# Kernel tuning notes

Measured on AMD Instinct MI355X. Metric: run time of the kernel, lower is better.

Reference implementation:

```python
import jax, jax.numpy as jnp
import numpy as np

B, S, H, I, G = 4, 2048, 2048, 8192, 128


def _onebit_quant(w, group_size):
    # Group-wise 1-bit (sign) quantization along the input dim with per-group
    # abs-mean scale, as in BitNet-style OneBitLinear.
    out_f, in_f = w.shape
    wg = w.reshape(out_f, in_f // group_size, group_size)
    scale = jnp.mean(jnp.abs(wg), axis=-1, keepdims=True)  # [out, n_groups, 1]
    wq = jnp.sign(wg) * scale
    return wq.reshape(out_f, in_f)


def setup_inputs() -> dict:
    key = jax.random.key(0)
    k1, k2, k3, k4 = jax.random.split(key, 4)
    return {
        "x": jax.random.normal(k1, (B, S, H), dtype=jnp.float32),
        "w_gate": jax.random.normal(k2, (I, H), dtype=jnp.float32) * 0.02,
        "w_up": jax.random.normal(k3, (I, H), dtype=jnp.float32) * 0.02,
        "w_down": jax.random.normal(k4, (H, I), dtype=jnp.float32) * 0.02,
        "group_size": G,
    }


def reference(x, w_gate, w_up, w_down, group_size):
    wg_q = _onebit_quant(w_gate, group_size)   # [I, H]
    wu_q = _onebit_quant(w_up, group_size)     # [I, H]
    wd_q = _onebit_quant(w_down, group_size)   # [H, I]
    gate = jnp.einsum('bsh,ih->bsi', x, wg_q)  # [B, S, I]
    up = jnp.einsum('bsh,ih->bsi', x, wu_q)    # [B, S, I]
    h = jax.nn.silu(gate) * up                 # [B, S, I]
    return jnp.einsum('bsi,hi->bsh', h, wd_q)  # [B, S, H]
```

## Files before the change

kernel.cpp:

```cpp
#include <hip/hip_runtime.h>
#include <hip/hip_bf16.h>
#include <cstdint>
#include <cstddef>

using bf16 = __hip_bfloat16;

typedef __attribute__((ext_vector_type(8))) short short8;
typedef __attribute__((ext_vector_type(4))) float f32x4;
typedef __attribute__((ext_vector_type(4))) unsigned short us4;

static constexpr int Bb = 4, Ss = 2048, Hh = 2048, Ii = 8192, Gg = 128;
static constexpr int Mm = Bb * Ss;

#define MEMFENCE() asm volatile("" ::: "memory")
#define BARRIER() do { MEMFENCE(); __builtin_amdgcn_s_barrier(); MEMFENCE(); } while (0)

__global__ void quant_onebit(const float* __restrict__ w, bf16* __restrict__ wq,
                             int ngroups) {
  int gid = blockIdx.x * 4 + (threadIdx.x >> 6);
  if (gid >= ngroups) return;
  int lane = threadIdx.x & 63;
  size_t base = (size_t)gid * Gg + (size_t)lane * 2;
  float2 v = *(const float2*)(w + base);
  float s = fabsf(v.x) + fabsf(v.y);
#pragma unroll
  for (int m = 32; m >= 1; m >>= 1) s += __shfl_xor(s, m);
  float scale = s * (1.0f / 128.0f);
  float q0 = (v.x > 0.f) ? scale : ((v.x < 0.f) ? -scale : 0.f);
  float q1 = (v.y > 0.f) ? scale : ((v.y < 0.f) ? -scale : 0.f);
  unsigned int p =
      (unsigned int)__builtin_bit_cast(unsigned short, __float2bfloat16(q0)) |
      ((unsigned int)__builtin_bit_cast(unsigned short, __float2bfloat16(q1)) << 16);
  *(unsigned int*)(wq + base) = p;
}

__global__ void cast_f32_bf16(const float* __restrict__ in, bf16* __restrict__ out,
                              size_t n4) {
  size_t i = (size_t)blockIdx.x * blockDim.x + threadIdx.x;
  if (i >= n4) return;
  float4 v = *(const float4*)(in + i * 4);
  us4 o;
  o.x = __builtin_bit_cast(unsigned short, __float2bfloat16(v.x));
  o.y = __builtin_bit_cast(unsigned short, __float2bfloat16(v.y));
  o.z = __builtin_bit_cast(unsigned short, __float2bfloat16(v.z));
  o.w = __builtin_bit_cast(unsigned short, __float2bfloat16(v.w));
  *(us4*)(out + i * 4) = o;
}

__device__ __forceinline__ void gload16(const bf16* g, char* l) {
  __builtin_amdgcn_global_load_lds(
      (const __attribute__((address_space(1))) void*)g,
      (__attribute__((address_space(3))) void*)l, 16, 0, 0);
}

__device__ __forceinline__ short8 lfrag(const char* part, int row, int s) {
  return *(const short8*)(part + row * 64 + (((s ^ (row >> 1)) & 3) << 4));
}

template <bool DUAL>
__global__ __launch_bounds__(512, 2)
void gemm_bt8(const bf16* __restrict__ A,
              const bf16* __restrict__ B0,
              const bf16* __restrict__ B1,
              bf16* __restrict__ OutBf,
              float* __restrict__ OutF,
              int M, int N, int K) {
  constexpr int BM = 256, BN = DUAL ? 128 : 256;
  constexpr int NF = DUAL ? 2 : 4;
  extern __shared__ char smem[];

  const int tid = threadIdx.x;
  const int wid = tid >> 6;
  const int lane = tid & 63;
  const int wr = wid >> 2;
  const int wc = wid & 3;
  const int lrow = lane & 15;
  const int ks = lane >> 4;

  const int nbx = N / BN;
  const int nwg = (int)gridDim.x;
  const int cpx = nwg >> 3;
  const int wg = (int)blockIdx.x;
  const int swz = (wg & 7) * cpx + (wg >> 3);
  const int m0 = (swz / nbx) * BM;
  const int n0 = (swz % nbx) * BN;

  const int NT = K / 64;

  const int srow = tid >> 2;
  const int slog8 = (((tid & 3) ^ ((tid >> 3) & 3)) << 3);
  const bf16* pA0 = A + (size_t)(m0 + srow) * K + slog8;
  const bf16* pA1 = pA0 + (size_t)128 * K;
  const bf16* pB0 = B0 + (size_t)(n0 + srow) * K + slog8;
  const bf16* pB1 = DUAL ? (B1 + (size_t)(n0 + srow) * K + slog8)
                         : (pB0 + (size_t)128 * K);
  const int dA = wid * 1024;

  auto stageA = [&](int t, int p) {
    char* b = smem + (size_t)(t & 1) * 65536 + p * 32768;
    const int koff = t * 64 + p * 32;
    gload16(pA0 + koff, b + dA);
    gload16(pA1 + koff, b + 8192 + dA);
  };
  auto stageB = [&](int t, int p) {
    char* b = smem + (size_t)(t & 1) * 65536 + p * 32768 + 16384;
    const int koff = t * 64 + p * 32;
    gload16(pB0 + koff, b + dA);
    gload16(pB1 + koff, b + 8192 + dA);
  };

  const f32x4 vzero = {0.f, 0.f, 0.f, 0.f};
  f32x4 acc0[8][NF];
  f32x4 acc1[DUAL ? 8 : 1][NF];
#pragma unroll
  for (int mf = 0; mf < 8; ++mf)
#pragma unroll
    for (int nf = 0; nf < NF; ++nf) {
      acc0[mf][nf] = vzero;
      if constexpr (DUAL) acc1[mf][nf] = vzero;
    }

  stageA(0, 0); stageB(0, 0);
  stageA(0, 1); stageB(0, 1);

  short8 fa[4], fb0[NF], fb1[DUAL ? NF : 1];

  for (int t = 0; t < NT; ++t) {
    const char* buf = smem + (size_t)(t & 1) * 65536;
#pragma unroll
    for (int p = 0; p < 2; ++p) {
      const char* Ap = buf + p * 32768;
      const char* Bp = Ap + 16384;

      if (p == 0 || t + 1 < NT)
        asm volatile("s_waitcnt vmcnt(4)" ::: "memory");
      else
        asm volatile("s_waitcnt vmcnt(0)" ::: "memory");
      BARRIER();
      if constexpr (DUAL) {
#pragma unroll
        for (int nf = 0; nf < 2; ++nf) {
          fb0[nf] = lfrag(Bp, wc * 32 + nf * 16 + lrow, ks);
          fb1[nf] = lfrag(Bp + 8192, wc * 32 + nf * 16 + lrow, ks);
        }
      } else {
#pragma unroll
        for (int nf = 0; nf < 4; ++nf)
          fb0[nf] = lfrag(Bp, wc * 64 + nf * 16 + lrow, ks);
      }
#pragma unroll
      for (int i = 0; i < 4; ++i)
        fa[i] = lfrag(Ap, wr * 128 + i * 16 + lrow, ks);
      if (t + 1 < NT) stageA(t + 1, p);
      __builtin_amdgcn_s_setprio(1);
#pragma unroll
      for (int i = 0; i < 4; ++i)
#pragma unroll
        for (int nf = 0; nf < NF; ++nf) {
          acc0[i][nf] = __builtin_amdgcn_mfma_f32_16x16x32_bf16(
              fa[i], fb0[nf], acc0[i][nf], 0, 0, 0);
          if constexpr (DUAL)
            acc1[i][nf] = __builtin_amdgcn_mfma_f32_16x16x32_bf16(
                fa[i], fb1[nf], acc1[i][nf], 0, 0, 0);
        }
      __builtin_amdgcn_s_setprio(0);
      BARRIER();

#pragma unroll
      for (int i = 0; i < 4; ++i)
        fa[i] = lfrag(Ap, wr * 128 + 64 + i * 16 + lrow, ks);
      if (t + 1 < NT) stageB(t + 1, p);
      __builtin_amdgcn_s_setprio(1);
#pragma unroll
      for (int i = 0; i < 4; ++i)
#pragma unroll
        for (int nf = 0; nf < NF; ++nf) {
          acc0[4 + i][nf] = __builtin_amdgcn_mfma_f32_16x16x32_bf16(
              fa[i], fb0[nf], acc0[4 + i][nf], 0, 0, 0);
          if constexpr (DUAL)
            acc1[4 + i][nf] = __builtin_amdgcn_mfma_f32_16x16x32_bf16(
                fa[i], fb1[nf], acc1[4 + i][nf], 0, 0, 0);
        }
      __builtin_amdgcn_s_setprio(0);
    }
  }

  const int crow0 = (lane >> 4) * 4;
  const int ccol = lane & 15;
#pragma unroll
  for (int mf = 0; mf < 8; ++mf)
#pragma unroll
    for (int nf = 0; nf < NF; ++nf)
#pragma unroll
      for (int j = 0; j < 4; ++j) {
        const int row = m0 + wr * 128 + mf * 16 + crow0 + j;
        if constexpr (DUAL) {
          const int col = n0 + wc * 32 + nf * 16 + ccol;
          float g = acc0[mf][nf][j];
          float u = acc1[mf][nf][j];
          OutBf[(size_t)row * N + col] =
              __float2bfloat16(g / (1.0f + expf(-g)) * u);
        } else {
          const int col = n0 + wc * 64 + nf * 16 + ccol;
          OutF[(size_t)row * N + col] = acc0[mf][nf][j];
        }
      }
}

extern "C" void kernel_launch(void* const* d_in, const int* in_sizes, int n_in,
                              void* d_out, int out_size, void* d_ws, size_t ws_size,
                              hipStream_t stream) {
  const float* x = (const float*)d_in[0];
  const float* wg = (const float*)d_in[1];
  const float* wu = (const float*)d_in[2];
  const float* wd = (const float*)d_in[3];
  float* out = (float*)d_out;

  char* ws = (char*)d_ws;
  bf16* xq = (bf16*)(ws + 0);
  bf16* wgq = (bf16*)(ws + (size_t)33554432);
  bf16* wuq = (bf16*)(ws + (size_t)67108864);
  bf16* hbuf = (bf16*)(ws + (size_t)100663296);
  bf16* wdq = xq;

  auto* kDual = gemm_bt8<true>;
  auto* kSingle = gemm_bt8<false>;
  (void)hipFuncSetAttribute((const void*)kDual,
                            hipFuncAttributeMaxDynamicSharedMemorySize, 131072);
  (void)hipFuncSetAttribute((const void*)kSingle,
                            hipFuncAttributeMaxDynamicSharedMemorySize, 131072);

  const int ngW = (Ii * Hh) / Gg;
  quant_onebit<<<ngW / 4, 256, 0, stream>>>(wg, wgq, ngW);
  quant_onebit<<<ngW / 4, 256, 0, stream>>>(wu, wuq, ngW);

  const size_t n4 = (size_t)Mm * Hh / 4;
  cast_f32_bf16<<<(unsigned)((n4 + 255) / 256), 256, 0, stream>>>(x, xq, n4);

  kDual<<<(Mm / 256) * (Ii / 128), 512, 131072, stream>>>(
      xq, wgq, wuq, hbuf, nullptr, Mm, Ii, Hh);

  quant_onebit<<<ngW / 4, 256, 0, stream>>>(wd, wdq, ngW);

  kSingle<<<(Mm / 256) * (Hh / 256), 512, 131072, stream>>>(
      hbuf, wdq, nullptr, nullptr, out, Mm, Hh, Ii);
}
```

Before: 842.9 us.

## Switch GEMM to 32x32x16 MFMA with k-sliced LDS staging

Replaces the 16x16x32 MFMA tiling with 32x32x16 MFMAs and re-lays out LDS staging into four k-slices of 16 per 64-wide K tile. Each slice is prefetched right after its fragments are read, using a single barrier per slice and counted vmcnt waits. The XOR swizzle on LDS rows is dropped. The aim is fewer LDS fragment reads per FLOP and a finer-grained load/compute pipeline, at the risk of LDS bank conflicts from the unswizzled 32-byte row layout and more barriers per K tile.

```diff
diff --git a/kernel.cpp b/kernel.cpp
--- a/kernel.cpp
+++ b/kernel.cpp
@@ -6,14 +6,13 @@
 using bf16 = __hip_bfloat16;
 
 typedef __attribute__((ext_vector_type(8))) short short8;
-typedef __attribute__((ext_vector_type(4))) float f32x4;
+typedef __attribute__((ext_vector_type(16))) float f32x16;
 typedef __attribute__((ext_vector_type(4))) unsigned short us4;
 
 static constexpr int Bb = 4, Ss = 2048, Hh = 2048, Ii = 8192, Gg = 128;
 static constexpr int Mm = Bb * Ss;
 
 #define MEMFENCE() asm volatile("" ::: "memory")
-#define BARRIER() do { MEMFENCE(); __builtin_amdgcn_s_barrier(); MEMFENCE(); } while (0)
 
 __global__ void quant_onebit(const float* __restrict__ w, bf16* __restrict__ wq,
                              int ngroups) {
@@ -53,10 +52,6 @@
       (__attribute__((address_space(3))) void*)l, 16, 0, 0);
 }
 
-__device__ __forceinline__ short8 lfrag(const char* part, int row, int s) {
-  return *(const short8*)(part + row * 64 + (((s ^ (row >> 1)) & 3) << 4));
-}
-
 template <bool DUAL>
 __global__ __launch_bounds__(512, 2)
 void gemm_bt8(const bf16* __restrict__ A,
@@ -66,7 +61,6 @@
               float* __restrict__ OutF,
               int M, int N, int K) {
   constexpr int BM = 256, BN = DUAL ? 128 : 256;
-  constexpr int NF = DUAL ? 2 : 4;
   extern __shared__ char smem[];
 
   const int tid = threadIdx.x;
@@ -74,8 +68,8 @@
   const int lane = tid & 63;
   const int wr = wid >> 2;
   const int wc = wid & 3;
-  const int lrow = lane & 15;
-  const int ks = lane >> 4;
+  const int l31 = lane & 31;
+  const int lh = lane >> 5;
 
   const int nbx = N / BN;
   const int nwg = (int)gridDim.x;
@@ -87,124 +81,89 @@
 
   const int NT = K / 64;
 
-  const int srow = tid >> 2;
-  const int slog8 = (((tid & 3) ^ ((tid >> 3) & 3)) << 3);
-  const bf16* pA0 = A + (size_t)(m0 + srow) * K + slog8;
-  const bf16* pA1 = pA0 + (size_t)128 * K;
-  const bf16* pB0 = B0 + (size_t)(n0 + srow) * K + slog8;
-  const bf16* pB1 = DUAL ? (B1 + (size_t)(n0 + srow) * K + slog8)
-                         : (pB0 + (size_t)128 * K);
-  const int dA = wid * 1024;
-
-  auto stageA = [&](int t, int p) {
-    char* b = smem + (size_t)(t & 1) * 65536 + p * 32768;
-    const int koff = t * 64 + p * 32;
-    gload16(pA0 + koff, b + dA);
-    gload16(pA1 + koff, b + 8192 + dA);
+  const int srow = tid >> 1;
+  const int se = (tid & 1) * 8;
+  const bf16* srcA = A + (size_t)(m0 + srow) * K + se;
+  const bf16* srcB;
+  if constexpr (DUAL)
+    srcB = (srow < 128 ? B0 + (size_t)(n0 + srow) * K
+                       : B1 + (size_t)(n0 + srow - 128) * K) + se;
+  else
+    srcB = B0 + (size_t)(n0 + srow) * K + se;
+  const int dOff = wid * 1024;
+
+  auto stage = [&](int t, int ks) {
+    const int koff = t * 64 + ks * 16;
+    char* base = smem + (size_t)(t & 1) * 65536 + ks * 8192;
+    gload16(srcA + koff, base + dOff);
+    gload16(srcB + koff, base + 32768 + dOff);
   };
-  auto stageB = [&](int t, int p) {
-    char* b = smem + (size_t)(t & 1) * 65536 + p * 32768 + 16384;
-    const int koff = t * 64 + p * 32;
-    gload16(pB0 + koff, b + dA);
-    gload16(pB1 + koff, b + 8192 + dA);
-  };
-
-  const f32x4 vzero = {0.f, 0.f, 0.f, 0.f};
-  f32x4 acc0[8][NF];
-  f32x4 acc1[DUAL ? 8 : 1][NF];
-#pragma unroll
-  for (int mf = 0; mf < 8; ++mf)
-#pragma unroll
-    for (int nf = 0; nf < NF; ++nf) {
-      acc0[mf][nf] = vzero;
-      if constexpr (DUAL) acc1[mf][nf] = vzero;
-    }
-
-  stageA(0, 0); stageB(0, 0);
-  stageA(0, 1); stageB(0, 1);
-
-  short8 fa[4], fb0[NF], fb1[DUAL ? NF : 1];
+
+  const int aOff = (wr * 128 + l31) * 32 + lh * 16;
+  const int bRow = DUAL ? (wc * 32 + l31) : (wc * 64 + l31);
+  const int bOff = bRow * 32 + lh * 16;
+  const int b1Off = DUAL ? 4096 : 1024;
+
+  const f32x16 vzero = {0.f};
+  f32x16 acc0[4], acc1[4];
+#pragma unroll
+  for (int mf = 0; mf < 4; ++mf) { acc0[mf] = vzero; acc1[mf] = vzero; }
+
+#pragma unroll
+  for (int ks = 0; ks < 4; ++ks) stage(0, ks);
+  asm volatile("s_waitcnt vmcnt(6)" ::: "memory");
+  __builtin_amdgcn_s_barrier();
+  MEMFENCE();
 
   for (int t = 0; t < NT; ++t) {
     const char* buf = smem + (size_t)(t & 1) * 65536;
 #pragma unroll
-    for (int p = 0; p < 2; ++p) {
-      const char* Ap = buf + p * 32768;
-      const char* Bp = Ap + 16384;
-
-      if (p == 0 || t + 1 < NT)
-        asm volatile("s_waitcnt vmcnt(4)" ::: "memory");
-      else
-        asm volatile("s_waitcnt vmcnt(0)" ::: "memory");
-      BARRIER();
-      if constexpr (DUAL) {
-#pragma unroll
-        for (int nf = 0; nf < 2; ++nf) {
-          fb0[nf] = lfrag(Bp, wc * 32 + nf * 16 + lrow, ks);
-          fb1[nf] = lfrag(Bp + 8192, wc * 32 + nf * 16 + lrow, ks);
-        }
-      } else {
-#pragma unroll
-        for (int nf = 0; nf < 4; ++nf)
-          fb0[nf] = lfrag(Bp, wc * 64 + nf * 16 + lrow, ks);
+    for (int ks = 0; ks < 4; ++ks) {
+      const char* As_ = buf + ks * 8192;
+      const char* Bs_ = buf + 32768 + ks * 8192;
+      short8 fa[4], fb0, fb1;
+#pragma unroll
+      for (int mf = 0; mf < 4; ++mf)
+        fa[mf] = *(const short8*)(As_ + aOff + mf * 1024);
+      fb0 = *(const short8*)(Bs_ + bOff);
+      fb1 = *(const short8*)(Bs_ + bOff + b1Off);
+      MEMFENCE();
+      if (t + 1 < NT) stage(t + 1, ks);
+      if (t + 1 < NT)     asm volatile("s_waitcnt vmcnt(6)" ::: "memory");
+      else if (ks == 0)   asm volatile("s_waitcnt vmcnt(4)" ::: "memory");
+      else if (ks == 1)   asm volatile("s_waitcnt vmcnt(2)" ::: "memory");
+      else if (ks == 2)   asm volatile("s_waitcnt vmcnt(0)" ::: "memory");
+      __builtin_amdgcn_s_barrier();
+      MEMFENCE();
+      __builtin_amdgcn_s_setprio(1);
+#pragma unroll
+      for (int mf = 0; mf < 4; ++mf) {
+        acc0[mf] = __builtin_amdgcn_mfma_f32_32x32x16_bf16(
+            fa[mf], fb0, acc0[mf], 0, 0, 0);
+        acc1[mf] = __builtin_amdgcn_mfma_f32_32x32x16_bf16(
+            fa[mf], fb1, acc1[mf], 0, 0, 0);
       }
-#pragma unroll
-      for (int i = 0; i < 4; ++i)
-        fa[i] = lfrag(Ap, wr * 128 + i * 16 + lrow, ks);
-      if (t + 1 < NT) stageA(t + 1, p);
-      __builtin_amdgcn_s_setprio(1);
-#pragma unroll
-      for (int i = 0; i < 4; ++i)
-#pragma unroll
-        for (int nf = 0; nf < NF; ++nf) {
-          acc0[i][nf] = __builtin_amdgcn_mfma_f32_16x16x32_bf16(
-              fa[i], fb0[nf], acc0[i][nf], 0, 0, 0);
-          if constexpr (DUAL)
-            acc1[i][nf] = __builtin_amdgcn_mfma_f32_16x16x32_bf16(
-                fa[i], fb1[nf], acc1[i][nf], 0, 0, 0);
-        }
-      __builtin_amdgcn_s_setprio(0);
-      BARRIER();
-
-#pragma unroll
-      for (int i = 0; i < 4; ++i)
-        fa[i] = lfrag(Ap, wr * 128 + 64 + i * 16 + lrow, ks);
-      if (t + 1 < NT) stageB(t + 1, p);
-      __builtin_amdgcn_s_setprio(1);
-#pragma unroll
-      for (int i = 0; i < 4; ++i)
-#pragma unroll
-        for (int nf = 0; nf < NF; ++nf) {
-          acc0[4 + i][nf] = __builtin_amdgcn_mfma_f32_16x16x32_bf16(
-              fa[i], fb0[nf], acc0[4 + i][nf], 0, 0, 0);
-          if constexpr (DUAL)
-            acc1[4 + i][nf] = __builtin_amdgcn_mfma_f32_16x16x32_bf16(
-                fa[i], fb1[nf], acc1[4 + i][nf], 0, 0, 0);
-        }
       __builtin_amdgcn_s_setprio(0);
     }
   }
 
-  const int crow0 = (lane >> 4) * 4;
-  const int ccol = lane & 15;
-#pragma unroll
-  for (int mf = 0; mf < 8; ++mf)
-#pragma unroll
-    for (int nf = 0; nf < NF; ++nf)
-#pragma unroll
-      for (int j = 0; j < 4; ++j) {
-        const int row = m0 + wr * 128 + mf * 16 + crow0 + j;
-        if constexpr (DUAL) {
-          const int col = n0 + wc * 32 + nf * 16 + ccol;
-          float g = acc0[mf][nf][j];
-          float u = acc1[mf][nf][j];
-          OutBf[(size_t)row * N + col] =
-              __float2bfloat16(g / (1.0f + expf(-g)) * u);
-        } else {
-          const int col = n0 + wc * 64 + nf * 16 + ccol;
-          OutF[(size_t)row * N + col] = acc0[mf][nf][j];
-        }
+#pragma unroll
+  for (int mf = 0; mf < 4; ++mf)
+#pragma unroll
+    for (int r = 0; r < 16; ++r) {
+      const int row = m0 + wr * 128 + mf * 32 + (r & 3) + 8 * (r >> 2) + 4 * lh;
+      if constexpr (DUAL) {
+        const int col = n0 + wc * 32 + l31;
+        float g = acc0[mf][r];
+        float u = acc1[mf][r];
+        OutBf[(size_t)row * N + col] =
+            __float2bfloat16(g / (1.0f + expf(-g)) * u);
+      } else {
+        const int col = n0 + wc * 64 + l31;
+        OutF[(size_t)row * N + col] = acc0[mf][r];
+        OutF[(size_t)row * N + col + 32] = acc1[mf][r];
       }
+    }
 }
 
 extern "C" void kernel_launch(void* const* d_in, const int* in_sizes, int n_in,
```

Result: slower. 1.076 ms (+27.7%).
